# Kernel tuning notes

Measured on AMD Instinct MI355X. Metric: run time of the kernel, lower is better.

## Reference

```python
import jax, jax.numpy as jnp
import numpy as np

N = 50000          # nodes
E = 800000         # edges (before self-loops)
F_IN = 256         # feature_dim
HEADS = 3
OUT = 128          # per-head channels
HO = HEADS * OUT   # 384
NUM_GRAPHS = 64
NUM_CLASSES = 2
SLOPE = 0.2        # PyG GATConv default negative_slope


def setup_inputs() -> dict:
    key = jax.random.key(0)
    ks = jax.random.split(key, 8)
    x = jax.random.normal(ks[0], (N, F_IN), dtype=jnp.float32)
    edge_index = jax.random.randint(ks[1], (2, E), 0, N)
    batch = jnp.sort(jax.random.randint(ks[2], (N,), 0, NUM_GRAPHS))
    # GATConv params (glorot-ish scales)
    W = jax.random.normal(ks[3], (F_IN, HO), dtype=jnp.float32) * (1.0 / np.sqrt(F_IN))
    att_src = jax.random.normal(ks[4], (HEADS, OUT), dtype=jnp.float32) * 0.1
    att_dst = jax.random.normal(ks[5], (HEADS, OUT), dtype=jnp.float32) * 0.1
    bias = jnp.zeros((HO,), dtype=jnp.float32)
    fc_w = jax.random.normal(ks[6], (HO, NUM_CLASSES), dtype=jnp.float32) * 0.05
    fc_b = jnp.zeros((NUM_CLASSES,), dtype=jnp.float32)
    return {"x": x, "edge_index": edge_index, "batch": batch, "W": W,
            "att_src": att_src, "att_dst": att_dst, "bias": bias,
            "fc_w": fc_w, "fc_b": fc_b}


def reference(x, edge_index, batch, W, att_src, att_dst, bias, fc_w, fc_b):
    n = x.shape[0]
    h = (x @ W).reshape(n, HEADS, OUT)                      # [N, H, C]
    # add self-loops (PyG default add_self_loops=True)
    loops = jnp.arange(n)
    src = jnp.concatenate([edge_index[0], loops])           # [E+N]
    dst = jnp.concatenate([edge_index[1], loops])
    # per-node attention logits
    a_src = jnp.einsum('nhc,hc->nh', h, att_src)            # [N, H]
    a_dst = jnp.einsum('nhc,hc->nh', h, att_dst)
    e = jax.nn.leaky_relu(a_src[src] + a_dst[dst], SLOPE)   # [E+N, H]
    # segment softmax over incoming edges of each dst node
    emax = jax.ops.segment_max(e, dst, num_segments=n)
    ex = jnp.exp(e - emax[dst])
    denom = jax.ops.segment_sum(ex, dst, num_segments=n)
    alpha = ex / (denom[dst] + 1e-16)                       # [E+N, H]
    # weighted scatter-add aggregation
    msg = h[src] * alpha[:, :, None]                        # [E+N, H, C]
    out = jax.ops.segment_sum(msg, dst, num_segments=n)     # [N, H, C]
    out = jax.nn.relu(out.reshape(n, HO) + bias)            # [N, 384]
    # global mean pool per graph
    counts = jax.ops.segment_sum(jnp.ones((n,), out.dtype), batch,
                                 num_segments=NUM_GRAPHS)
    pooled = jax.ops.segment_sum(out, batch, num_segments=NUM_GRAPHS)
    pooled = pooled / jnp.maximum(counts, 1.0)[:, None]     # [G, 384]
    return pooled @ fc_w + fc_b                             # [G, num_classes]
```

## Files before the change

### kernel.cpp

```cpp
#include <hip/hip_runtime.h>
#include <hip/hip_bf16.h>
#include <math.h>

#define HEADS 3
#define HO 384
#define NGRAPH 64
#define F_IN 256
#define SLOPE 0.2f

typedef __attribute__((ext_vector_type(8))) short bf8;
typedef __attribute__((ext_vector_type(4))) float f4;

__device__ __forceinline__ unsigned short bfr(float f) {
    unsigned u = __float_as_uint(f);
    u += 0x7fffu + ((u >> 16) & 1u);
    return (unsigned short)(u >> 16);
}
__device__ __forceinline__ float bflo(unsigned u) { return __uint_as_float(u << 16); }
__device__ __forceinline__ float bfhi(unsigned u) { return __uint_as_float(u & 0xffff0000u); }
__device__ __forceinline__ float lrelu(float v) { return (v > 0.f) ? v : SLOPE * v; }

__global__ __launch_bounds__(256) void misc_k(const int* __restrict__ ei,
                                              const float* __restrict__ W,
                                              const int* __restrict__ batch,
                                              int* __restrict__ count,
                                              int* __restrict__ rank,
                                              short* __restrict__ WbT,
                                              int* __restrict__ gstart,
                                              int NBc, int E, int N) {
    int b = blockIdx.x;
    if (b < NBc) {
        int e = b * 256 + threadIdx.x;
        int ET = E + N;
        if (e >= ET) return;
        int d = (e < E) ? ei[E + e] : (e - E);
        rank[e] = atomicAdd(&count[d], 1);
    } else if (b < NBc + 384) {
        int n = b - NBc;
        int k = threadIdx.x;
        WbT[n * 256 + k] = (short)bfr(W[(size_t)k * HO + n]);
    } else {
        int g = threadIdx.x;
        if (g > NGRAPH) return;
        int lo = 0, hi = N;
        while (lo < hi) { int mid = (lo + hi) >> 1; if (batch[mid] < g) lo = mid + 1; else hi = mid; }
        gstart[g] = lo;
    }
}

#define XS_STRIDE 40
__global__ __launch_bounds__(256, 3) void gemm_att(const float* __restrict__ X,
                                                   const short* __restrict__ WbT,
                                                   const float* __restrict__ att_src,
                                                   const float* __restrict__ att_dst,
                                                   unsigned* __restrict__ Hb,
                                                   float* __restrict__ aSrcO,
                                                   float* __restrict__ aDstO, int N) {
    __shared__ short Xs[64 * XS_STRIDE];
    __shared__ short Bs[384 * XS_STRIDE];
    __shared__ float lsS[64][8];
    __shared__ float lsD[64][8];
    int t = threadIdx.x;
    int w = t >> 6, lane = t & 63;
    int quad = lane >> 4, l15 = lane & 15;
    int rbase = blockIdx.x * 64;

    int sr = t >> 2;
    int sko = (t & 3) * 8;
    int xrow = rbase + sr;
    xrow = (xrow < N) ? xrow : (N - 1);
    const float* xrp = X + (size_t)xrow * F_IN;

    f4 acc[4][6] = {};

    float4 p0 = *(const float4*)(xrp + sko);
    float4 p1 = *(const float4*)(xrp + sko + 4);

    for (int k0 = 0; k0 < F_IN; k0 += 32) {
        __syncthreads();
        {
            bf8 pk;
            pk[0] = (short)bfr(p0.x); pk[1] = (short)bfr(p0.y);
            pk[2] = (short)bfr(p0.z); pk[3] = (short)bfr(p0.w);
            pk[4] = (short)bfr(p1.x); pk[5] = (short)bfr(p1.y);
            pk[6] = (short)bfr(p1.z); pk[7] = (short)bfr(p1.w);
            *(bf8*)(&Xs[sr * XS_STRIDE + sko]) = pk;
        }
#pragma unroll
        for (int i = 0; i < 6; i++) {
            int n = i * 64 + sr;
            bf8 b = *(const bf8*)(WbT + (size_t)n * F_IN + k0 + sko);
            *(bf8*)(&Bs[n * XS_STRIDE + sko]) = b;
        }
        __syncthreads();
        if (k0 + 32 < F_IN) {
            p0 = *(const float4*)(xrp + k0 + 32 + sko);
            p1 = *(const float4*)(xrp + k0 + 32 + sko + 4);
        }
        bf8 ar[4], br[6];
#pragma unroll
        for (int at = 0; at < 4; at++)
            ar[at] = *(const bf8*)(&Xs[(at * 16 + l15) * XS_STRIDE + quad * 8]);
#pragma unroll
        for (int nt = 0; nt < 6; nt++)
            br[nt] = *(const bf8*)(&Bs[(w * 96 + nt * 16 + l15) * XS_STRIDE + quad * 8]);
#pragma unroll
        for (int at = 0; at < 4; at++)
#pragma unroll
            for (int nt = 0; nt < 6; nt++)
                acc[at][nt] = __builtin_amdgcn_mfma_f32_16x16x32_bf16(ar[at], br[nt], acc[at][nt], 0, 0, 0);
    }

    const int splits[4] = {6, 2, 4, 0};
    int split = splits[w];
    float asv[6], adv[6];
#pragma unroll
    for (int nt = 0; nt < 6; nt++) {
        int c = w * 96 + nt * 16 + l15;
        asv[nt] = att_src[c];
        adv[nt] = att_dst[c];
    }
#pragma unroll
    for (int at = 0; at < 4; at++) {
#pragma unroll
        for (int r = 0; r < 4; r++) {
            float paS = 0.f, pbS = 0.f, paD = 0.f, pbD = 0.f;
#pragma unroll
            for (int nt = 0; nt < 6; nt++) {
                float v = acc[at][nt][r];
                if (nt < split) { paS += v * asv[nt]; paD += v * adv[nt]; }
                else            { pbS += v * asv[nt]; pbD += v * adv[nt]; }
            }
#pragma unroll
            for (int off = 1; off < 16; off <<= 1) {
                paS += __shfl_xor(paS, off); pbS += __shfl_xor(pbS, off);
                paD += __shfl_xor(paD, off); pbD += __shfl_xor(pbD, off);
            }
            if (l15 == 0) {
                int row = at * 16 + quad * 4 + r;
                lsS[row][w * 2 + 0] = paS; lsS[row][w * 2 + 1] = pbS;
                lsD[row][w * 2 + 0] = paD; lsD[row][w * 2 + 1] = pbD;
            }
        }
    }
#pragma unroll
    for (int at = 0; at < 4; at++) {
#pragma unroll
        for (int nt = 0; nt < 6; nt++) {
#pragma unroll
            for (int r = 0; r < 4; r++) {
                float v = acc[at][nt][r];
                float vp = __shfl_xor(v, 1);
                int node = rbase + at * 16 + quad * 4 + r;
                if (!(lane & 1) && node < N) {
                    unsigned pk = (unsigned)bfr(v) | ((unsigned)bfr(vp) << 16);
                    Hb[(size_t)node * 192 + w * 48 + nt * 8 + (l15 >> 1)] = pk;
                }
            }
        }
    }
    __syncthreads();
    if (t < 64) {
        int node = rbase + t;
        if (node < N) {
            aSrcO[node * 3 + 0] = lsS[t][0] + lsS[t][2];
            aSrcO[node * 3 + 1] = lsS[t][3] + lsS[t][4];
            aSrcO[node * 3 + 2] = lsS[t][5] + lsS[t][7];
            aDstO[node * 3 + 0] = lsD[t][0] + lsD[t][2];
            aDstO[node * 3 + 1] = lsD[t][3] + lsD[t][4];
            aDstO[node * 3 + 2] = lsD[t][5] + lsD[t][7];
        }
    }
}

__global__ __launch_bounds__(256) void scan_a(const int* __restrict__ count,
                                              int* __restrict__ offsets,
                                              int* __restrict__ bsums, int N) {
    __shared__ int tmp[256];
    int t = threadIdx.x;
    int i = blockIdx.x * 256 + t;
    int v = (i < N) ? count[i] : 0;
    tmp[t] = v;
    __syncthreads();
    for (int off = 1; off < 256; off <<= 1) {
        int x = (t >= off) ? tmp[t - off] : 0;
        __syncthreads();
        tmp[t] += x;
        __syncthreads();
    }
    if (i < N) offsets[i] = tmp[t] - v;
    if (t == 255) bsums[blockIdx.x] = tmp[255];
}

__global__ __launch_bounds__(256) void scan_b(int* __restrict__ bsums, int NB) {
    __shared__ int tmp[256];
    int t = threadIdx.x;
    int v = (t < NB) ? bsums[t] : 0;
    tmp[t] = v;
    __syncthreads();
    for (int off = 1; off < 256; off <<= 1) {
        int x = (t >= off) ? tmp[t - off] : 0;
        __syncthreads();
        tmp[t] += x;
        __syncthreads();
    }
    if (t < NB) bsums[t] = tmp[t] - v;
}

__global__ __launch_bounds__(256) void scan_c(int* __restrict__ offsets,
                                              const int* __restrict__ bsums, int N) {
    int i = blockIdx.x * 256 + threadIdx.x;
    if (i < N) offsets[i] += bsums[blockIdx.x];
}

__global__ __launch_bounds__(256) void scatter_k(const int* __restrict__ ei,
                                                 const int* __restrict__ rank,
                                                 const int* __restrict__ offsets,
                                                 int* __restrict__ csr_src, int E, int N) {
    int e = blockIdx.x * 256 + threadIdx.x;
    int ET = E + N;
    if (e >= ET) return;
    int s, d;
    if (e < E) { s = ei[e]; d = ei[E + e]; } else { s = e - E; d = s; }
    csr_src[offsets[d] + rank[e]] = s;
}

__global__ __launch_bounds__(256) void aggregate_k(const unsigned* __restrict__ Hb,
                                                   const int* __restrict__ csr_src,
                                                   const int* __restrict__ offsets,
                                                   const int* __restrict__ count,
                                                   const float* __restrict__ a_src,
                                                   const float* __restrict__ a_dst,
                                                   const float* __restrict__ bias,
                                                   unsigned* __restrict__ outb, int N) {
    int wid = blockIdx.x * 4 + (threadIdx.x >> 6);
    int lane = threadIdx.x & 63;
    if (wid >= N) return;
    int start = offsets[wid], n = count[wid];
    float ad0 = a_dst[wid * 3 + 0], ad1 = a_dst[wid * 3 + 1], ad2 = a_dst[wid * 3 + 2];
    float a0l = 0.f, a0h = 0.f, a1l = 0.f, a1h = 0.f, a2l = 0.f, a2h = 0.f;

    if (n <= 64) {
        int sreg = 0;
        float l0 = -INFINITY, l1 = -INFINITY, l2 = -INFINITY;
        if (lane < n) {
            sreg = csr_src[start + lane];
            l0 = lrelu(a_src[sreg * 3 + 0] + ad0);
            l1 = lrelu(a_src[sreg * 3 + 1] + ad1);
            l2 = lrelu(a_src[sreg * 3 + 2] + ad2);
        }
        float m0 = l0, m1 = l1, m2 = l2;
#pragma unroll
        for (int off = 1; off < 64; off <<= 1) {
            m0 = fmaxf(m0, __shfl_xor(m0, off));
            m1 = fmaxf(m1, __shfl_xor(m1, off));
            m2 = fmaxf(m2, __shfl_xor(m2, off));
        }
        float e0 = (lane < n) ? expf(l0 - m0) : 0.f;
        float e1 = (lane < n) ? expf(l1 - m1) : 0.f;
        float e2 = (lane < n) ? expf(l2 - m2) : 0.f;
        float s0 = e0, s1 = e1, s2 = e2;
#pragma unroll
        for (int off = 1; off < 64; off <<= 1) {
            s0 += __shfl_xor(s0, off);
            s1 += __shfl_xor(s1, off);
            s2 += __shfl_xor(s2, off);
        }
        float w0r = e0 / (s0 + 1e-16f);
        float w1r = e1 / (s1 + 1e-16f);
        float w2r = e2 / (s2 + 1e-16f);
        int j = 0;
        for (; j + 8 <= n; j += 8) {
            int idx[8];
#pragma unroll
            for (int q = 0; q < 8; q++) idx[q] = __shfl(sreg, j + q);
            unsigned u0[8], u1[8], u2[8];
#pragma unroll
            for (int q = 0; q < 8; q++) {
                const unsigned* h = Hb + (size_t)idx[q] * 192;
                u0[q] = h[lane]; u1[q] = h[lane + 64]; u2[q] = h[lane + 128];
            }
#pragma unroll
            for (int q = 0; q < 8; q++) {
                float wq0 = __shfl(w0r, j + q);
                float wq1 = __shfl(w1r, j + q);
                float wq2 = __shfl(w2r, j + q);
                a0l += wq0 * bflo(u0[q]); a0h += wq0 * bfhi(u0[q]);
                a1l += wq1 * bflo(u1[q]); a1h += wq1 * bfhi(u1[q]);
                a2l += wq2 * bflo(u2[q]); a2h += wq2 * bfhi(u2[q]);
            }
        }
        for (; j < n; j++) {
            int si = __shfl(sreg, j);
            const unsigned* h = Hb + (size_t)si * 192;
            unsigned u0 = h[lane], u1 = h[lane + 64], u2 = h[lane + 128];
            float w0 = __shfl(w0r, j), w1 = __shfl(w1r, j), w2 = __shfl(w2r, j);
            a0l += w0 * bflo(u0); a0h += w0 * bfhi(u0);
            a1l += w1 * bflo(u1); a1h += w1 * bfhi(u1);
            a2l += w2 * bflo(u2); a2h += w2 * bfhi(u2);
        }
    } else {
        float m0 = -INFINITY, m1 = -INFINITY, m2 = -INFINITY;
        for (int j = lane; j < n; j += 64) {
            int s = csr_src[start + j];
            m0 = fmaxf(m0, lrelu(a_src[s * 3 + 0] + ad0));
            m1 = fmaxf(m1, lrelu(a_src[s * 3 + 1] + ad1));
            m2 = fmaxf(m2, lrelu(a_src[s * 3 + 2] + ad2));
        }
#pragma unroll
        for (int off = 1; off < 64; off <<= 1) {
            m0 = fmaxf(m0, __shfl_xor(m0, off));
            m1 = fmaxf(m1, __shfl_xor(m1, off));
            m2 = fmaxf(m2, __shfl_xor(m2, off));
        }
        float s0 = 0.f, s1 = 0.f, s2 = 0.f;
        for (int j = lane; j < n; j += 64) {
            int s = csr_src[start + j];
            s0 += expf(lrelu(a_src[s * 3 + 0] + ad0) - m0);
            s1 += expf(lrelu(a_src[s * 3 + 1] + ad1) - m1);
            s2 += expf(lrelu(a_src[s * 3 + 2] + ad2) - m2);
        }
#pragma unroll
        for (int off = 1; off < 64; off <<= 1) {
            s0 += __shfl_xor(s0, off);
            s1 += __shfl_xor(s1, off);
            s2 += __shfl_xor(s2, off);
        }
        float i0 = 1.f / (s0 + 1e-16f), i1 = 1.f / (s1 + 1e-16f), i2 = 1.f / (s2 + 1e-16f);
        for (int j = 0; j < n; j++) {
            int s = csr_src[start + j];
            float w0 = expf(lrelu(a_src[s * 3 + 0] + ad0) - m0) * i0;
            float w1 = expf(lrelu(a_src[s * 3 + 1] + ad1) - m1) * i1;
            float w2 = expf(lrelu(a_src[s * 3 + 2] + ad2) - m2) * i2;
            const unsigned* h = Hb + (size_t)s * 192;
            unsigned u0 = h[lane], u1 = h[lane + 64], u2 = h[lane + 128];
            a0l += w0 * bflo(u0); a0h += w0 * bfhi(u0);
            a1l += w1 * bflo(u1); a1h += w1 * bfhi(u1);
            a2l += w2 * bflo(u2); a2h += w2 * bfhi(u2);
        }
    }

    unsigned* orow = outb + (size_t)wid * 192;
    int c0 = 2 * lane;
    float b0 = bias[c0], b1 = bias[c0 + 1];
    float b2 = bias[128 + c0], b3 = bias[128 + c0 + 1];
    float b4 = bias[256 + c0], b5 = bias[256 + c0 + 1];
    float v, x0, x1;
    unsigned pk;
    v = a0l + b0; x0 = (v > 0.f) ? v : 0.f;
    v = a0h + b1; x1 = (v > 0.f) ? v : 0.f;
    pk = (unsigned)bfr(x0) | ((unsigned)bfr(x1) << 16);
    orow[lane] = pk;
    v = a1l + b2; x0 = (v > 0.f) ? v : 0.f;
    v = a1h + b3; x1 = (v > 0.f) ? v : 0.f;
    pk = (unsigned)bfr(x0) | ((unsigned)bfr(x1) << 16);
    orow[64 + lane] = pk;
    v = a2l + b4; x0 = (v > 0.f) ? v : 0.f;
    v = a2h + b5; x1 = (v > 0.f) ? v : 0.f;
    pk = (unsigned)bfr(x0) | ((unsigned)bfr(x1) << 16);
    orow[128 + lane] = pk;
}

__global__ __launch_bounds__(192) void pool_k(const unsigned* __restrict__ outb,
                                              const int* __restrict__ gstart,
                                              float* __restrict__ pooled) {
    int g = blockIdx.x;
    int chunk = blockIdx.y;
    int t = threadIdx.x;
    int lo = gstart[g], hi = gstart[g + 1];
    float al = 0.f, ah = 0.f;
    for (int r = lo + chunk; r < hi; r += 8) {
        unsigned u = outb[(size_t)r * 192 + t];
        al += bflo(u);
        ah += bfhi(u);
    }
    atomicAdd(&pooled[g * HO + 2 * t], al);
    atomicAdd(&pooled[g * HO + 2 * t + 1], ah);
}

__global__ __launch_bounds__(64) void fc_k(const float* __restrict__ pooled,
                                           const int* __restrict__ gstart,
                                           const float* __restrict__ fc_w,
                                           const float* __restrict__ fc_b,
                                           float* __restrict__ out) {
    int g = blockIdx.x;
    int lane = threadIdx.x;
    float a0 = 0.f, a1 = 0.f;
#pragma unroll
    for (int k = 0; k < 6; k++) {
        int c = lane + 64 * k;
        float pv = pooled[g * HO + c];
        a0 += pv * fc_w[c * 2 + 0];
        a1 += pv * fc_w[c * 2 + 1];
    }
#pragma unroll
    for (int off = 32; off > 0; off >>= 1) {
        a0 += __shfl_down(a0, off);
        a1 += __shfl_down(a1, off);
    }
    if (lane == 0) {
        float cnt = fmaxf((float)(gstart[g + 1] - gstart[g]), 1.0f);
        out[g * 2 + 0] = a0 / cnt + fc_b[0];
        out[g * 2 + 1] = a1 / cnt + fc_b[1];
    }
}

extern "C" void kernel_launch(void* const* d_in, const int* in_sizes, int n_in,
                              void* d_out, int out_size, void* d_ws, size_t ws_size,
                              hipStream_t stream) {
    const float* x       = (const float*)d_in[0];
    const int*   ei      = (const int*)d_in[1];
    const int*   batch   = (const int*)d_in[2];
    const float* W       = (const float*)d_in[3];
    const float* att_src = (const float*)d_in[4];
    const float* att_dst = (const float*)d_in[5];
    const float* bias    = (const float*)d_in[6];
    const float* fc_w    = (const float*)d_in[7];
    const float* fc_b    = (const float*)d_in[8];
    float* out = (float*)d_out;

    const int N = in_sizes[2];
    const int E = in_sizes[1] / 2;
    const int ET = E + N;

    char* p = (char*)d_ws;
    auto alloc = [&](size_t bytes) -> char* {
        char* r = p;
        p += (bytes + 255) & ~(size_t)255;
        return r;
    };
    short*    wbt    = (short*)alloc((size_t)HO * F_IN * 2);
    unsigned* hb     = (unsigned*)alloc((size_t)N * 192 * 4);
    unsigned* outb   = (unsigned*)alloc((size_t)N * 192 * 4);
    float*    a_src  = (float*)alloc((size_t)N * 3 * 4);
    float*    a_dst  = (float*)alloc((size_t)N * 3 * 4);
    char*     zstart = p;
    int*      count  = (int*)alloc((size_t)N * 4);
    float*    pooled = (float*)alloc((size_t)NGRAPH * HO * 4);
    size_t    zbytes = (size_t)(p - zstart);
    int*      offsets = (int*)alloc((size_t)N * 4);
    int*      rank    = (int*)alloc((size_t)ET * 4);
    int*      bsums   = (int*)alloc(4096);
    int*      gstart  = (int*)alloc(1024);
    int*      csr_src = (int*)alloc((size_t)ET * 4);

    hipMemsetAsync(zstart, 0, zbytes, stream);

    int NBc = (ET + 255) / 256;
    misc_k<<<NBc + 384 + 1, 256, 0, stream>>>(ei, W, batch, count, rank, wbt, gstart,
                                              NBc, E, N);
    gemm_att<<<(N + 63) / 64, 256, 0, stream>>>(x, wbt, att_src, att_dst,
                                                hb, a_src, a_dst, N);
    int NB = (N + 255) / 256;
    scan_a<<<NB, 256, 0, stream>>>(count, offsets, bsums, N);
    scan_b<<<1, 256, 0, stream>>>(bsums, NB);
    scan_c<<<NB, 256, 0, stream>>>(offsets, bsums, N);
    scatter_k<<<(ET + 255) / 256, 256, 0, stream>>>(ei, rank, offsets, csr_src, E, N);
    aggregate_k<<<(N + 3) / 4, 256, 0, stream>>>(hb, csr_src, offsets, count,
                                                 a_src, a_dst, bias, outb, N);
    dim3 pg(NGRAPH, 8);
    pool_k<<<pg, 192, 0, stream>>>(outb, gstart, pooled);
    fc_k<<<NGRAPH, 64, 0, stream>>>(pooled, gstart, fc_w, fc_b, out);

    (void)n_in; (void)out_size; (void)ws_size;
}
```

Before: 329.7 us.

## Restructure GEMM to 8 waves with register-direct weight loads and double-buffered X tile

The projection GEMM now uses 512-thread blocks with 8 waves, each owning 48 output columns. Each wave loads its weight fragments directly from global memory into registers, prefetched one step ahead, so the 384-row shared-memory B tile is gone. The X tile is double-buffered in shared memory, which halves the barriers per k-step, and the attention-logit reduction is remapped to the new head splits. The scan_c kernel is also removed by adding the block prefix sum inside the scatter and aggregate kernels. The trade-off is more global and L2 traffic for weights, since there is no shared-memory reuse across waves, plus a slightly more complex offset lookup.

```diff
diff --git a/kernel.cpp b/kernel.cpp
--- a/kernel.cpp
+++ b/kernel.cpp
@@ -48,75 +48,82 @@
     }
 }
 
-#define XS_STRIDE 40
-__global__ __launch_bounds__(256, 3) void gemm_att(const float* __restrict__ X,
+#define XST 40
+__global__ __launch_bounds__(512, 4) void gemm_att(const float* __restrict__ X,
                                                    const short* __restrict__ WbT,
                                                    const float* __restrict__ att_src,
                                                    const float* __restrict__ att_dst,
                                                    unsigned* __restrict__ Hb,
                                                    float* __restrict__ aSrcO,
                                                    float* __restrict__ aDstO, int N) {
-    __shared__ short Xs[64 * XS_STRIDE];
-    __shared__ short Bs[384 * XS_STRIDE];
-    __shared__ float lsS[64][8];
-    __shared__ float lsD[64][8];
+    __shared__ short Xs[2][64 * XST];
+    __shared__ float lsS[64][16];
+    __shared__ float lsD[64][16];
     int t = threadIdx.x;
     int w = t >> 6, lane = t & 63;
     int quad = lane >> 4, l15 = lane & 15;
     int rbase = blockIdx.x * 64;
 
-    int sr = t >> 2;
-    int sko = (t & 3) * 8;
+    int sr = t >> 3;
+    int kq = (t & 7) * 4;
     int xrow = rbase + sr;
     xrow = (xrow < N) ? xrow : (N - 1);
     const float* xrp = X + (size_t)xrow * F_IN;
 
-    f4 acc[4][6] = {};
-
-    float4 p0 = *(const float4*)(xrp + sko);
-    float4 p1 = *(const float4*)(xrp + sko + 4);
-
-    for (int k0 = 0; k0 < F_IN; k0 += 32) {
-        __syncthreads();
-        {
-            bf8 pk;
-            pk[0] = (short)bfr(p0.x); pk[1] = (short)bfr(p0.y);
-            pk[2] = (short)bfr(p0.z); pk[3] = (short)bfr(p0.w);
-            pk[4] = (short)bfr(p1.x); pk[5] = (short)bfr(p1.y);
-            pk[6] = (short)bfr(p1.z); pk[7] = (short)bfr(p1.w);
-            *(bf8*)(&Xs[sr * XS_STRIDE + sko]) = pk;
-        }
-#pragma unroll
-        for (int i = 0; i < 6; i++) {
-            int n = i * 64 + sr;
-            bf8 b = *(const bf8*)(WbT + (size_t)n * F_IN + k0 + sko);
-            *(bf8*)(&Bs[n * XS_STRIDE + sko]) = b;
-        }
-        __syncthreads();
-        if (k0 + 32 < F_IN) {
-            p0 = *(const float4*)(xrp + k0 + 32 + sko);
-            p1 = *(const float4*)(xrp + k0 + 32 + sko + 4);
-        }
-        bf8 ar[4], br[6];
+    const short* wrow[3];
+#pragma unroll
+    for (int nt = 0; nt < 3; nt++)
+        wrow[nt] = WbT + (size_t)(w * 48 + nt * 16 + l15) * F_IN + quad * 8;
+
+    f4 acc[4][3] = {};
+
+    {
+        float4 xc = *(const float4*)(xrp + kq);
+        unsigned lo = (unsigned)bfr(xc.x) | ((unsigned)bfr(xc.y) << 16);
+        unsigned hi = (unsigned)bfr(xc.z) | ((unsigned)bfr(xc.w) << 16);
+        *(uint2*)(&Xs[0][sr * XST + kq]) = make_uint2(lo, hi);
+    }
+    bf8 bcur[3];
+#pragma unroll
+    for (int nt = 0; nt < 3; nt++) bcur[nt] = *(const bf8*)(wrow[nt]);
+    __syncthreads();
+
+    for (int c = 0; c < 8; c++) {
+        int buf = c & 1;
+        float4 xn;
+        bf8 bnext[3];
+        if (c < 7) {
+            int k1 = (c + 1) * 32;
+            xn = *(const float4*)(xrp + k1 + kq);
+#pragma unroll
+            for (int nt = 0; nt < 3; nt++)
+                bnext[nt] = *(const bf8*)(wrow[nt] + k1);
+        }
+        bf8 ar[4];
 #pragma unroll
         for (int at = 0; at < 4; at++)
-            ar[at] = *(const bf8*)(&Xs[(at * 16 + l15) * XS_STRIDE + quad * 8]);
-#pragma unroll
-        for (int nt = 0; nt < 6; nt++)
-            br[nt] = *(const bf8*)(&Bs[(w * 96 + nt * 16 + l15) * XS_STRIDE + quad * 8]);
+            ar[at] = *(const bf8*)(&Xs[buf][(at * 16 + l15) * XST + quad * 8]);
 #pragma unroll
         for (int at = 0; at < 4; at++)
 #pragma unroll
-            for (int nt = 0; nt < 6; nt++)
-                acc[at][nt] = __builtin_amdgcn_mfma_f32_16x16x32_bf16(ar[at], br[nt], acc[at][nt], 0, 0, 0);
-    }
-
-    const int splits[4] = {6, 2, 4, 0};
-    int split = splits[w];
-    float asv[6], adv[6];
-#pragma unroll
-    for (int nt = 0; nt < 6; nt++) {
-        int c = w * 96 + nt * 16 + l15;
+            for (int nt = 0; nt < 3; nt++)
+                acc[at][nt] = __builtin_amdgcn_mfma_f32_16x16x32_bf16(ar[at], bcur[nt], acc[at][nt], 0, 0, 0);
+        if (c < 7) {
+            unsigned lo = (unsigned)bfr(xn.x) | ((unsigned)bfr(xn.y) << 16);
+            unsigned hi = (unsigned)bfr(xn.z) | ((unsigned)bfr(xn.w) << 16);
+            *(uint2*)(&Xs[buf ^ 1][sr * XST + kq]) = make_uint2(lo, hi);
+            __syncthreads();
+#pragma unroll
+            for (int nt = 0; nt < 3; nt++) bcur[nt] = bnext[nt];
+        }
+    }
+
+    const int splitT[8] = {3, 3, 2, 3, 3, 1, 3, 3};
+    int split = splitT[w];
+    float asv[3], adv[3];
+#pragma unroll
+    for (int nt = 0; nt < 3; nt++) {
+        int c = w * 48 + nt * 16 + l15;
         asv[nt] = att_src[c];
         adv[nt] = att_dst[c];
     }
@@ -126,7 +133,7 @@
         for (int r = 0; r < 4; r++) {
             float paS = 0.f, pbS = 0.f, paD = 0.f, pbD = 0.f;
 #pragma unroll
-            for (int nt = 0; nt < 6; nt++) {
+            for (int nt = 0; nt < 3; nt++) {
                 float v = acc[at][nt][r];
                 if (nt < split) { paS += v * asv[nt]; paD += v * adv[nt]; }
                 else            { pbS += v * asv[nt]; pbD += v * adv[nt]; }
@@ -146,7 +153,7 @@
 #pragma unroll
     for (int at = 0; at < 4; at++) {
 #pragma unroll
-        for (int nt = 0; nt < 6; nt++) {
+        for (int nt = 0; nt < 3; nt++) {
 #pragma unroll
             for (int r = 0; r < 4; r++) {
                 float v = acc[at][nt][r];
@@ -154,7 +161,7 @@
                 int node = rbase + at * 16 + quad * 4 + r;
                 if (!(lane & 1) && node < N) {
                     unsigned pk = (unsigned)bfr(v) | ((unsigned)bfr(vp) << 16);
-                    Hb[(size_t)node * 192 + w * 48 + nt * 8 + (l15 >> 1)] = pk;
+                    Hb[(size_t)node * 192 + w * 24 + nt * 8 + (l15 >> 1)] = pk;
                 }
             }
         }
@@ -163,12 +170,12 @@
     if (t < 64) {
         int node = rbase + t;
         if (node < N) {
-            aSrcO[node * 3 + 0] = lsS[t][0] + lsS[t][2];
-            aSrcO[node * 3 + 1] = lsS[t][3] + lsS[t][4];
-            aSrcO[node * 3 + 2] = lsS[t][5] + lsS[t][7];
-            aDstO[node * 3 + 0] = lsD[t][0] + lsD[t][2];
-            aDstO[node * 3 + 1] = lsD[t][3] + lsD[t][4];
-            aDstO[node * 3 + 2] = lsD[t][5] + lsD[t][7];
+            aSrcO[node * 3 + 0] = lsS[t][0] + lsS[t][2] + lsS[t][4];
+            aSrcO[node * 3 + 1] = lsS[t][5] + lsS[t][6] + lsS[t][8] + lsS[t][10];
+            aSrcO[node * 3 + 2] = lsS[t][11] + lsS[t][12] + lsS[t][14];
+            aDstO[node * 3 + 0] = lsD[t][0] + lsD[t][2] + lsD[t][4];
+            aDstO[node * 3 + 1] = lsD[t][5] + lsD[t][6] + lsD[t][8] + lsD[t][10];
+            aDstO[node * 3 + 2] = lsD[t][11] + lsD[t][12] + lsD[t][14];
         }
     }
 }
@@ -207,27 +214,23 @@
     if (t < NB) bsums[t] = tmp[t] - v;
 }
 
-__global__ __launch_bounds__(256) void scan_c(int* __restrict__ offsets,
-                                              const int* __restrict__ bsums, int N) {
-    int i = blockIdx.x * 256 + threadIdx.x;
-    if (i < N) offsets[i] += bsums[blockIdx.x];
-}
-
 __global__ __launch_bounds__(256) void scatter_k(const int* __restrict__ ei,
                                                  const int* __restrict__ rank,
                                                  const int* __restrict__ offsets,
+                                                 const int* __restrict__ bsums,
                                                  int* __restrict__ csr_src, int E, int N) {
     int e = blockIdx.x * 256 + threadIdx.x;
     int ET = E + N;
     if (e >= ET) return;
     int s, d;
     if (e < E) { s = ei[e]; d = ei[E + e]; } else { s = e - E; d = s; }
-    csr_src[offsets[d] + rank[e]] = s;
+    csr_src[offsets[d] + bsums[d >> 8] + rank[e]] = s;
 }
 
 __global__ __launch_bounds__(256) void aggregate_k(const unsigned* __restrict__ Hb,
                                                    const int* __restrict__ csr_src,
                                                    const int* __restrict__ offsets,
+                                                   const int* __restrict__ bsums,
                                                    const int* __restrict__ count,
                                                    const float* __restrict__ a_src,
                                                    const float* __restrict__ a_dst,
@@ -236,7 +239,8 @@
     int wid = blockIdx.x * 4 + (threadIdx.x >> 6);
     int lane = threadIdx.x & 63;
     if (wid >= N) return;
-    int start = offsets[wid], n = count[wid];
+    int start = offsets[wid] + bsums[wid >> 8];
+    int n = count[wid];
     float ad0 = a_dst[wid * 3 + 0], ad1 = a_dst[wid * 3 + 1], ad2 = a_dst[wid * 3 + 2];
     float a0l = 0.f, a0h = 0.f, a1l = 0.f, a1h = 0.f, a2l = 0.f, a2h = 0.f;
 
@@ -449,14 +453,13 @@
     int NBc = (ET + 255) / 256;
     misc_k<<<NBc + 384 + 1, 256, 0, stream>>>(ei, W, batch, count, rank, wbt, gstart,
                                               NBc, E, N);
-    gemm_att<<<(N + 63) / 64, 256, 0, stream>>>(x, wbt, att_src, att_dst,
+    gemm_att<<<(N + 63) / 64, 512, 0, stream>>>(x, wbt, att_src, att_dst,
                                                 hb, a_src, a_dst, N);
     int NB = (N + 255) / 256;
     scan_a<<<NB, 256, 0, stream>>>(count, offsets, bsums, N);
     scan_b<<<1, 256, 0, stream>>>(bsums, NB);
-    scan_c<<<NB, 256, 0, stream>>>(offsets, bsums, N);
-    scatter_k<<<(ET + 255) / 256, 256, 0, stream>>>(ei, rank, offsets, csr_src, E, N);
-    aggregate_k<<<(N + 3) / 4, 256, 0, stream>>>(hb, csr_src, offsets, count,
+    scatter_k<<<(ET + 255) / 256, 256, 0, stream>>>(ei, rank, offsets, bsums, csr_src, E, N);
+    aggregate_k<<<(N + 3) / 4, 256, 0, stream>>>(hb, csr_src, offsets, bsums, count,
                                                  a_src, a_dst, bias, outb, N);
     dim3 pg(NGRAPH, 8);
     pool_k<<<pg, 192, 0, stream>>>(outb, gstart, pooled);
```

Result: no change. 330.5 us (+0.2%).
